# Kernel optimization log

Measured on AMD Instinct MI355X. Metric: run time of the kernel, lower is better.

## Reference

```python
import jax, jax.numpy as jnp
import numpy as np

B, N, F_IN, H, D = 2, 3000, 64, 4, 32
NEG = -1e9  # mask value used by the original layer

def setup_inputs() -> dict:
    key = jax.random.key(0)
    ks = jax.random.split(key, 6)
    h = jax.random.normal(ks[0], (B, N, F_IN), dtype=jnp.float32)
    # dense 0/1 adjacency
    a = jax.random.randint(ks[1], (B, N, N), 0, 2).astype(jnp.float32)
    kernel = jax.random.normal(ks[2], (H, F_IN, D), dtype=jnp.float32) * 0.1
    att_k1 = jax.random.normal(ks[3], (H, D), dtype=jnp.float32) * 0.1
    att_k2 = jax.random.normal(ks[4], (H, D), dtype=jnp.float32) * 0.1
    bias = jax.random.normal(ks[5], (H, D), dtype=jnp.float32) * 0.1
    return {"h": h, "a": a, "kernel": kernel, "att_k1": att_k1, "att_k2": att_k2, "bias": bias}

def reference(h, a, kernel, att_k1, att_k2, bias):
    # per-head projection: [B,H,N,D]
    feat = jnp.einsum('bnf,hfd->bhnd', h, kernel)
    e1 = jnp.einsum('bhnd,hd->bhn', feat, att_k1)  # attention (query part)
    e2 = jnp.einsum('bhnd,hd->bhn', feat, att_k2)  # attention_2 (key part)
    # dense branch: att = a * (e1_i + e2_j); NO LeakyReLU in dense path (faithful)
    adj = a[:, None]                                   # [B,1,N,N]
    scores = adj * (e1[..., :, None] + e2[..., None, :])
    scores = scores + jnp.where(adj == 0, jnp.float32(NEG), jnp.float32(0))
    att = jax.nn.softmax(scores, axis=-1)
    att = att * (adj != 0).astype(att.dtype)
    # dropout is identity at inference
    out = jnp.einsum('bhnm,bhmd->bhnd', att, feat)
    out = out + bias[None, :, None, :]
    out = jax.nn.relu(out)
    # zero out all-zero input nodes
    node_mask = (jnp.sum((h != 0).astype(jnp.float32), axis=-1, keepdims=True) > 0).astype(jnp.float32)  # [B,N,1]
    out = out * node_mask[:, None]
    # concat heads -> [B,N,H*D]
    return out.transpose(0, 2, 1, 3).reshape(h.shape[0], h.shape[1], -1)
```

## Files before the change

### kernel.cpp

```cpp
#include <hip/hip_runtime.h>
#include <hip/hip_bf16.h>
#include <stdint.h>

#define B_ 2
#define N_ 3000
#define F_ 64
#define H_ 4
#define D_ 32
#define K_ 128
#define KT_ 9
#define NCHP_ 96
#define BITSW_ 96
#define NROWT_ 188
#define NRG_ 47
#define S_ 8
#define CHB_ 9216
#define PTB_ 9216

typedef short bf16x8 __attribute__((ext_vector_type(8)));
typedef float f32x4  __attribute__((ext_vector_type(4)));

__device__ __forceinline__ unsigned short f2bf(float f) {
    uint32_t x = __float_as_uint(f);
    return (unsigned short)((x + 0x7FFFu + ((x >> 16) & 1u)) >> 16);
}

__global__ void k_bits(const float* __restrict__ a, uint32_t* __restrict__ bits) {
    int b = blockIdx.x / N_;
    int n = blockIdx.x % N_;
    const float* row = a + (size_t)(b * N_ + n) * N_;
    uint32_t* brow = bits + (size_t)(b * N_ + n) * BITSW_;
    int wv = threadIdx.x >> 6, lane = threadIdx.x & 63;
    for (int it = 0; it < 12; ++it) {
        int ig = wv * 12 + it;
        if (ig < 47) {
            int m = ig * 64 + lane;
            float v = (m < N_) ? row[m] : 0.f;
            unsigned long long bal = __ballot(v != 0.f);
            if (lane == 0)  brow[ig * 2]     = (uint32_t)bal;
            if (lane == 32) brow[ig * 2 + 1] = (uint32_t)(bal >> 32);
        }
    }
    if (threadIdx.x == 0) { brow[94] = 0u; brow[95] = 0u; }
}

__global__ void k_feat(const float* __restrict__ hin, const float* __restrict__ kern,
                       const float* __restrict__ ak2,
                       float* __restrict__ feat, float* __restrict__ e2,
                       float* __restrict__ nmask) {
    int b = blockIdx.x / N_;
    int n = blockIdx.x % N_;
    __shared__ float hrow[F_];
    int tid = threadIdx.x;
    if (tid < F_) hrow[tid] = hin[(size_t)(b * N_ + n) * F_ + tid];
    __syncthreads();
    int hh = tid >> 5, d = tid & 31;
    float acc = 0.f;
    #pragma unroll
    for (int f = 0; f < F_; ++f)
        acc = fmaf(hrow[f], kern[(hh * F_ + f) * D_ + d], acc);
    feat[((size_t)(b * H_ + hh) * N_ + n) * D_ + d] = acc;
    float v = acc * ak2[hh * D_ + d];
    #pragma unroll
    for (int o = 16; o >= 1; o >>= 1) v += __shfl_xor(v, o, 32);
    if (d == 0) e2[(size_t)(b * H_ + hh) * N_ + n] = v;
    unsigned long long bal = __ballot(tid < F_ && hrow[tid & (F_ - 1)] != 0.0f);
    if (tid == 0) nmask[b * N_ + n] = (bal != 0ull) ? 1.0f : 0.0f;
}

__global__ void k_G(const float* __restrict__ feat, const float* __restrict__ e2,
                    bf16x8* __restrict__ G) {
    int idx = blockIdx.x * blockDim.x + threadIdx.x;
    const int total = B_ * NCHP_ * KT_ * 64;
    if (idx >= total) return;
    int lane = idx & 63;
    int t  = (idx >> 6) % KT_;
    int ch = ((idx >> 6) / KT_) % NCHP_;
    int b  = idx / (64 * KT_ * NCHP_);
    int rg = lane >> 4, col = lane & 15;
    int k  = t * 16 + col;
    int m0 = ch * 32 + rg * 8;
    float vals[8];
    if (k < K_ + H_) {
        int hh, d; bool wonly;
        if (k < K_) { hh = k >> 5; d = k & 31; wonly = false; }
        else        { hh = k - K_; d = 0;      wonly = true;  }
        const float* e2p = e2 + (size_t)(b * H_ + hh) * N_;
        const float* fp  = feat + (size_t)(b * H_ + hh) * N_ * D_ + d;
        #pragma unroll
        for (int j = 0; j < 8; ++j) {
            int m = m0 + j;
            float v = 0.f;
            if (m < N_) {
                float w = __expf(e2p[m]);
                v = wonly ? w : w * fp[(size_t)m * D_];
            }
            vals[j] = v;
        }
    } else {
        #pragma unroll
        for (int j = 0; j < 8; ++j) vals[j] = 0.f;
    }
    union { bf16x8 v; unsigned short u[8]; } o;
    #pragma unroll
    for (int j = 0; j < 8; ++j) o.u[j] = f2bf(vals[j]);
    G[idx] = o.v;
}

__device__ __forceinline__ void g2lds16(const void* g, void* l) {
    __builtin_amdgcn_global_load_lds(
        (const __attribute__((address_space(1))) void*)g,
        (__attribute__((address_space(3))) void*)l, 16, 0, 0);
}

__device__ __forceinline__ void stage9(const char* src_ln, char* dst, int w) {
    int t0 = 2 * w * 1024;
    g2lds16(src_ln + t0,        dst + t0);
    g2lds16(src_ln + t0 + 1024, dst + t0 + 1024);
    if (w == 3) g2lds16(src_ln + 8 * 1024, dst + 8 * 1024);
}

__device__ __forceinline__ void compute9(const char* gb, uint32_t word, int rg,
                                         f32x4 (&acc)[KT_]) {
    uint32_t mb = (word >> (rg * 8)) & 0xFFu;
    union { uint32_t u[4]; bf16x8 v; } af;
    af.u[0] = ((mb & 1u)   ? 0x3F80u : 0u) | ((mb & 2u)   ? 0x3F800000u : 0u);
    af.u[1] = ((mb & 4u)   ? 0x3F80u : 0u) | ((mb & 8u)   ? 0x3F800000u : 0u);
    af.u[2] = ((mb & 16u)  ? 0x3F80u : 0u) | ((mb & 32u)  ? 0x3F800000u : 0u);
    af.u[3] = ((mb & 64u)  ? 0x3F80u : 0u) | ((mb & 128u) ? 0x3F800000u : 0u);
    #pragma unroll
    for (int t = 0; t < KT_; ++t) {
        bf16x8 g = *(const bf16x8*)(gb + t * 1024);
        acc[t] = __builtin_amdgcn_mfma_f32_16x16x32_bf16(af.v, g, acc[t], 0, 0, 0);
    }
}

__global__ void __launch_bounds__(256, 4) k_main(
        const uint32_t* __restrict__ bits, const bf16x8* __restrict__ G,
        float* __restrict__ partial) {
    int bid = blockIdx.x;
    int s    = bid % S_;
    int rg64 = (bid / S_) % NRG_;
    int b    = bid / (S_ * NRG_);
    int w = threadIdx.x >> 6;
    int l = threadIdx.x & 63;
    int rg = l >> 4, col = l & 15;
    int row = min(rg64 * 64 + w * 16 + col, N_ - 1);
    const uint32_t* brow = bits + (size_t)(b * N_ + row) * BITSW_ + s * 12;
    const char* Gsrc = (const char*)G + ((size_t)(b * NCHP_ + s * 12)) * CHB_ + (size_t)l * 16;

    __shared__ __align__(16) char Gbuf[2][CHB_];

    f32x4 acc[KT_];
    #pragma unroll
    for (int t = 0; t < KT_; ++t) acc[t] = (f32x4){0.f, 0.f, 0.f, 0.f};

    uint32_t bw[12];
    #pragma unroll
    for (int i = 0; i < 12; ++i) bw[i] = brow[i];

    stage9(Gsrc, Gbuf[0], w);
    __syncthreads();

    #pragma unroll
    for (int i = 0; i < 12; ++i) {
        if (i + 1 < 12) stage9(Gsrc + (size_t)(i + 1) * CHB_, Gbuf[(i + 1) & 1], w);
        compute9(Gbuf[i & 1] + l * 16, bw[i], rg, acc);
        __syncthreads();
    }

    float* pw = partial + (size_t)bid * PTB_ + w * (KT_ * 256);
    #pragma unroll
    for (int t = 0; t < KT_; ++t)
        #pragma unroll
        for (int r = 0; r < 4; ++r)
            pw[t * 256 + r * 64 + l] = acc[t][r];
}

__global__ void __launch_bounds__(256) k_red(
        const float* __restrict__ partial, const float* __restrict__ bias,
        const float* __restrict__ nmask, float* __restrict__ out) {
    int rt = blockIdx.x % NROWT_;
    int b  = blockIdx.x / NROWT_;
    int nbase = rt * 16;
    int rg64  = rt >> 2;
    int wslot = rt & 3;
    int tid = threadIdx.x;
    __shared__ float sm[KT_ * 256];
    const float* pbase = partial + (size_t)((b * NRG_ + rg64) * S_) * PTB_ + wslot * (KT_ * 256);
    #pragma unroll
    for (int k = 0; k < 9; ++k) {
        int flat = tid + k * 256;
        float s = 0.f;
        #pragma unroll
        for (int sp = 0; sp < S_; ++sp) s += pbase[(size_t)sp * PTB_ + flat];
        sm[flat] = s;
    }
    __syncthreads();
    #pragma unroll
    for (int k = 0; k < 9; ++k) {
        int flat = tid + k * 256;
        if (flat < 2048) {
            int t4r = flat >> 6;
            int t = t4r >> 2, r = t4r & 3;
            int lane = flat & 63;
            int rg = lane >> 4, col = lane & 15;
            int rowi = rg * 4 + r;
            int n = nbase + rowi;
            if (n < N_) {
                int hh = t >> 1;
                int r2 = rowi & 3, rg2 = rowi >> 2;
                float den = sm[(32 + r2) * 64 + (rg2 << 4) + hh];
                float v = (den > 0.f) ? sm[flat] / den : 0.f;
                v += bias[t * 16 + col];
                v = fmaxf(v, 0.f);
                v *= nmask[b * N_ + n];
                out[(size_t)(b * N_ + n) * K_ + t * 16 + col] = v;
            }
        }
    }
}

extern "C" void kernel_launch(void* const* d_in, const int* in_sizes, int n_in,
                              void* d_out, int out_size, void* d_ws, size_t ws_size,
                              hipStream_t stream) {
    const float* h    = (const float*)d_in[0];
    const float* a    = (const float*)d_in[1];
    const float* kern = (const float*)d_in[2];
    const float* ak2  = (const float*)d_in[4];
    const float* bias = (const float*)d_in[5];
    float* out = (float*)d_out;

    char* ws = (char*)d_ws;
    size_t o_feat  = 0;
    size_t o_e2    = o_feat  + 3072000;
    size_t o_nmask = o_e2    + 96000;
    size_t o_bits  = o_nmask + 24064;
    size_t o_G     = o_bits  + 2304000;
    size_t o_part  = o_G     + 1769472;
    float*    feat  = (float*)(ws + o_feat);
    float*    e2    = (float*)(ws + o_e2);
    float*    nmask = (float*)(ws + o_nmask);
    uint32_t* bits  = (uint32_t*)(ws + o_bits);
    bf16x8*   G     = (bf16x8*)(ws + o_G);
    float*    part  = (float*)(ws + o_part);

    k_bits<<<dim3(B_ * N_), dim3(256), 0, stream>>>(a, bits);
    k_feat<<<dim3(B_ * N_), dim3(128), 0, stream>>>(h, kern, ak2, feat, e2, nmask);
    int gtot = B_ * NCHP_ * KT_ * 64;
    k_G   <<<dim3((gtot + 255) / 256), dim3(256), 0, stream>>>(feat, e2, G);
    k_main<<<dim3(B_ * NRG_ * S_), dim3(256), 0, stream>>>(bits, G, part);
    k_red <<<dim3(B_ * NROWT_), dim3(256), 0, stream>>>(part, bias, nmask, out);
}
```

Before: 58.28 us.

## Drop LDS staging in k_main; split MFMA tiles across two waves with register double-buffering

The main masked-aggregation kernel stops staging G chunks in shared memory through global_load_lds and block-wide barriers. Each 128-thread block now handles one 16-row tile with a 4-way K split instead of 8. Its two waves divide the nine output tiles (5 and 4) and double-buffer G directly in registers. This removes the barrier and LDS traffic but duplicates G global reads across row tiles, since there are now many more blocks reading the same G. The partial layout and the reducer are changed to match.

```diff
diff --git a/kernel.cpp b/kernel.cpp
--- a/kernel.cpp
+++ b/kernel.cpp
@@ -12,10 +12,9 @@
 #define NCHP_ 96
 #define BITSW_ 96
 #define NROWT_ 188
-#define NRG_ 47
-#define S_ 8
+#define S4_ 4
+#define PT_ 2304
 #define CHB_ 9216
-#define PTB_ 9216
 
 typedef short bf16x8 __attribute__((ext_vector_type(8)));
 typedef float f32x4  __attribute__((ext_vector_type(4)));
@@ -107,21 +106,15 @@
     G[idx] = o.v;
 }
 
-__device__ __forceinline__ void g2lds16(const void* g, void* l) {
-    __builtin_amdgcn_global_load_lds(
-        (const __attribute__((address_space(1))) void*)g,
-        (__attribute__((address_space(3))) void*)l, 16, 0, 0);
-}
-
-__device__ __forceinline__ void stage9(const char* src_ln, char* dst, int w) {
-    int t0 = 2 * w * 1024;
-    g2lds16(src_ln + t0,        dst + t0);
-    g2lds16(src_ln + t0 + 1024, dst + t0 + 1024);
-    if (w == 3) g2lds16(src_ln + 8 * 1024, dst + 8 * 1024);
-}
-
-__device__ __forceinline__ void compute9(const char* gb, uint32_t word, int rg,
-                                         f32x4 (&acc)[KT_]) {
+template<int NT>
+__device__ __forceinline__ void loadG(const char* p, bf16x8 (&g)[NT]) {
+    #pragma unroll
+    for (int t = 0; t < NT; ++t) g[t] = *(const bf16x8*)(p + t * 1024);
+}
+
+template<int NT>
+__device__ __forceinline__ void computeG(uint32_t word, int rg,
+                                         const bf16x8 (&g)[NT], f32x4 (&acc)[NT]) {
     uint32_t mb = (word >> (rg * 8)) & 0xFFu;
     union { uint32_t u[4]; bf16x8 v; } af;
     af.u[0] = ((mb & 1u)   ? 0x3F80u : 0u) | ((mb & 2u)   ? 0x3F800000u : 0u);
@@ -129,52 +122,55 @@
     af.u[2] = ((mb & 16u)  ? 0x3F80u : 0u) | ((mb & 32u)  ? 0x3F800000u : 0u);
     af.u[3] = ((mb & 64u)  ? 0x3F80u : 0u) | ((mb & 128u) ? 0x3F800000u : 0u);
     #pragma unroll
-    for (int t = 0; t < KT_; ++t) {
-        bf16x8 g = *(const bf16x8*)(gb + t * 1024);
-        acc[t] = __builtin_amdgcn_mfma_f32_16x16x32_bf16(af.v, g, acc[t], 0, 0, 0);
-    }
-}
-
-__global__ void __launch_bounds__(256, 4) k_main(
+    for (int t = 0; t < NT; ++t)
+        acc[t] = __builtin_amdgcn_mfma_f32_16x16x32_bf16(af.v, g[t], acc[t], 0, 0, 0);
+}
+
+template<int T0, int NT>
+__device__ __forceinline__ void waverun(const char* GsT, const uint32_t (&bw)[24],
+                                        int rg, float* pout, int l) {
+    f32x4 acc[NT];
+    #pragma unroll
+    for (int t = 0; t < NT; ++t) acc[t] = (f32x4){0.f, 0.f, 0.f, 0.f};
+    bf16x8 gA[NT], gB[NT];
+    loadG<NT>(GsT, gA);
+    #pragma unroll
+    for (int i = 0; i < 24; ++i) {
+        if ((i & 1) == 0) {
+            if (i + 1 < 24) loadG<NT>(GsT + (size_t)(i + 1) * CHB_, gB);
+            computeG<NT>(bw[i], rg, gA, acc);
+        } else {
+            if (i + 1 < 24) loadG<NT>(GsT + (size_t)(i + 1) * CHB_, gA);
+            computeG<NT>(bw[i], rg, gB, acc);
+        }
+    }
+    #pragma unroll
+    for (int t = 0; t < NT; ++t)
+        #pragma unroll
+        for (int r = 0; r < 4; ++r)
+            pout[(T0 + t) * 256 + r * 64 + l] = acc[t][r];
+}
+
+__global__ void __launch_bounds__(128, 4) k_main(
         const uint32_t* __restrict__ bits, const bf16x8* __restrict__ G,
         float* __restrict__ partial) {
     int bid = blockIdx.x;
-    int s    = bid % S_;
-    int rg64 = (bid / S_) % NRG_;
-    int b    = bid / (S_ * NRG_);
+    int s  = bid & 3;
+    int rt = (bid >> 2) % NROWT_;
+    int b  = bid / (S4_ * NROWT_);
     int w = threadIdx.x >> 6;
     int l = threadIdx.x & 63;
     int rg = l >> 4, col = l & 15;
-    int row = min(rg64 * 64 + w * 16 + col, N_ - 1);
-    const uint32_t* brow = bits + (size_t)(b * N_ + row) * BITSW_ + s * 12;
-    const char* Gsrc = (const char*)G + ((size_t)(b * NCHP_ + s * 12)) * CHB_ + (size_t)l * 16;
-
-    __shared__ __align__(16) char Gbuf[2][CHB_];
-
-    f32x4 acc[KT_];
-    #pragma unroll
-    for (int t = 0; t < KT_; ++t) acc[t] = (f32x4){0.f, 0.f, 0.f, 0.f};
-
-    uint32_t bw[12];
-    #pragma unroll
-    for (int i = 0; i < 12; ++i) bw[i] = brow[i];
-
-    stage9(Gsrc, Gbuf[0], w);
-    __syncthreads();
-
-    #pragma unroll
-    for (int i = 0; i < 12; ++i) {
-        if (i + 1 < 12) stage9(Gsrc + (size_t)(i + 1) * CHB_, Gbuf[(i + 1) & 1], w);
-        compute9(Gbuf[i & 1] + l * 16, bw[i], rg, acc);
-        __syncthreads();
-    }
-
-    float* pw = partial + (size_t)bid * PTB_ + w * (KT_ * 256);
-    #pragma unroll
-    for (int t = 0; t < KT_; ++t)
-        #pragma unroll
-        for (int r = 0; r < 4; ++r)
-            pw[t * 256 + r * 64 + l] = acc[t][r];
+    int row = min(rt * 16 + col, N_ - 1);
+    const uint4* bq = (const uint4*)(bits + (size_t)(b * N_ + row) * BITSW_ + s * 24);
+    uint4 b0 = bq[0], b1 = bq[1], b2 = bq[2], b3 = bq[3], b4 = bq[4], b5 = bq[5];
+    uint32_t bw[24] = { b0.x, b0.y, b0.z, b0.w,  b1.x, b1.y, b1.z, b1.w,
+                        b2.x, b2.y, b2.z, b2.w,  b3.x, b3.y, b3.z, b3.w,
+                        b4.x, b4.y, b4.z, b4.w,  b5.x, b5.y, b5.z, b5.w };
+    const char* Gs = (const char*)G + (size_t)(b * NCHP_ + s * 24) * CHB_ + (size_t)l * 16;
+    float* pout = partial + (size_t)bid * PT_;
+    if (w == 0) waverun<0, 5>(Gs,            bw, rg, pout, l);
+    else        waverun<5, 4>(Gs + 5 * 1024, bw, rg, pout, l);
 }
 
 __global__ void __launch_bounds__(256) k_red(
@@ -183,17 +179,15 @@
     int rt = blockIdx.x % NROWT_;
     int b  = blockIdx.x / NROWT_;
     int nbase = rt * 16;
-    int rg64  = rt >> 2;
-    int wslot = rt & 3;
     int tid = threadIdx.x;
-    __shared__ float sm[KT_ * 256];
-    const float* pbase = partial + (size_t)((b * NRG_ + rg64) * S_) * PTB_ + wslot * (KT_ * 256);
+    __shared__ float sm[PT_];
+    const float* pbase = partial + (size_t)((b * NROWT_ + rt) * S4_) * PT_;
     #pragma unroll
     for (int k = 0; k < 9; ++k) {
         int flat = tid + k * 256;
         float s = 0.f;
         #pragma unroll
-        for (int sp = 0; sp < S_; ++sp) s += pbase[(size_t)sp * PTB_ + flat];
+        for (int sp = 0; sp < S4_; ++sp) s += pbase[(size_t)sp * PT_ + flat];
         sm[flat] = s;
     }
     __syncthreads();
@@ -249,6 +243,6 @@
     k_feat<<<dim3(B_ * N_), dim3(128), 0, stream>>>(h, kern, ak2, feat, e2, nmask);
     int gtot = B_ * NCHP_ * KT_ * 64;
     k_G   <<<dim3((gtot + 255) / 256), dim3(256), 0, stream>>>(feat, e2, G);
-    k_main<<<dim3(B_ * NRG_ * S_), dim3(256), 0, stream>>>(bits, G, part);
+    k_main<<<dim3(B_ * NROWT_ * S4_), dim3(128), 0, stream>>>(bits, G, part);
     k_red <<<dim3(B_ * NROWT_), dim3(256), 0, stream>>>(part, bias, nmask, out);
 }
```

Result: slower. 68.09 us (+16.8%).

## Fuse adjacency bitmask construction into main MFMA kernel and refine LDS pipeline waits

Applied to the files above, without the earlier changes.

Removes the separate k_bits pass: each k_main block now reads its own 64-row by 384-column slice of the dense adjacency, ballots it into a shared-memory bit table, and uses that directly. This drops a kernel launch and the write and re-read of the bits buffer. The double-buffered LDS staging loop now uses explicit vmcnt waits and raw s_barriers so the next chunk's load can overlap the current compute. Occupancy is lowered to 2 blocks per CU, and the block's adjacency read is serialized ahead of compute, which could expose memory latency.

```diff
diff --git a/kernel.cpp b/kernel.cpp
--- a/kernel.cpp
+++ b/kernel.cpp
@@ -10,7 +10,6 @@
 #define K_ 128
 #define KT_ 9
 #define NCHP_ 96
-#define BITSW_ 96
 #define NROWT_ 188
 #define NRG_ 47
 #define S_ 8
@@ -23,25 +22,6 @@
 __device__ __forceinline__ unsigned short f2bf(float f) {
     uint32_t x = __float_as_uint(f);
     return (unsigned short)((x + 0x7FFFu + ((x >> 16) & 1u)) >> 16);
-}
-
-__global__ void k_bits(const float* __restrict__ a, uint32_t* __restrict__ bits) {
-    int b = blockIdx.x / N_;
-    int n = blockIdx.x % N_;
-    const float* row = a + (size_t)(b * N_ + n) * N_;
-    uint32_t* brow = bits + (size_t)(b * N_ + n) * BITSW_;
-    int wv = threadIdx.x >> 6, lane = threadIdx.x & 63;
-    for (int it = 0; it < 12; ++it) {
-        int ig = wv * 12 + it;
-        if (ig < 47) {
-            int m = ig * 64 + lane;
-            float v = (m < N_) ? row[m] : 0.f;
-            unsigned long long bal = __ballot(v != 0.f);
-            if (lane == 0)  brow[ig * 2]     = (uint32_t)bal;
-            if (lane == 32) brow[ig * 2 + 1] = (uint32_t)(bal >> 32);
-        }
-    }
-    if (threadIdx.x == 0) { brow[94] = 0u; brow[95] = 0u; }
 }
 
 __global__ void k_feat(const float* __restrict__ hin, const float* __restrict__ kern,
@@ -113,31 +93,18 @@
         (__attribute__((address_space(3))) void*)l, 16, 0, 0);
 }
 
-__device__ __forceinline__ void stage9(const char* src_ln, char* dst, int w) {
+__device__ __forceinline__ void stage_chunk(const char* src_ln, char* dst, int w) {
     int t0 = 2 * w * 1024;
     g2lds16(src_ln + t0,        dst + t0);
     g2lds16(src_ln + t0 + 1024, dst + t0 + 1024);
-    if (w == 3) g2lds16(src_ln + 8 * 1024, dst + 8 * 1024);
-}
-
-__device__ __forceinline__ void compute9(const char* gb, uint32_t word, int rg,
-                                         f32x4 (&acc)[KT_]) {
-    uint32_t mb = (word >> (rg * 8)) & 0xFFu;
-    union { uint32_t u[4]; bf16x8 v; } af;
-    af.u[0] = ((mb & 1u)   ? 0x3F80u : 0u) | ((mb & 2u)   ? 0x3F800000u : 0u);
-    af.u[1] = ((mb & 4u)   ? 0x3F80u : 0u) | ((mb & 8u)   ? 0x3F800000u : 0u);
-    af.u[2] = ((mb & 16u)  ? 0x3F80u : 0u) | ((mb & 32u)  ? 0x3F800000u : 0u);
-    af.u[3] = ((mb & 64u)  ? 0x3F80u : 0u) | ((mb & 128u) ? 0x3F800000u : 0u);
-    #pragma unroll
-    for (int t = 0; t < KT_; ++t) {
-        bf16x8 g = *(const bf16x8*)(gb + t * 1024);
-        acc[t] = __builtin_amdgcn_mfma_f32_16x16x32_bf16(af.v, g, acc[t], 0, 0, 0);
-    }
-}
-
-__global__ void __launch_bounds__(256, 4) k_main(
-        const uint32_t* __restrict__ bits, const bf16x8* __restrict__ G,
+    if (w == 3) g2lds16(src_ln + 8192, dst + 8192);
+}
+
+__global__ void __launch_bounds__(256, 2) k_main(
+        const float* __restrict__ a, const bf16x8* __restrict__ G,
         float* __restrict__ partial) {
+    __shared__ __align__(16) bf16x8 Gbuf[2][KT_ * 64];
+    __shared__ uint32_t bitw[64][13];
     int bid = blockIdx.x;
     int s    = bid % S_;
     int rg64 = (bid / S_) % NRG_;
@@ -145,28 +112,60 @@
     int w = threadIdx.x >> 6;
     int l = threadIdx.x & 63;
     int rg = l >> 4, col = l & 15;
-    int row = min(rg64 * 64 + w * 16 + col, N_ - 1);
-    const uint32_t* brow = bits + (size_t)(b * N_ + row) * BITSW_ + s * 12;
-    const char* Gsrc = (const char*)G + ((size_t)(b * NCHP_ + s * 12)) * CHB_ + (size_t)l * 16;
-
-    __shared__ __align__(16) char Gbuf[2][CHB_];
+
+    for (int r = 0; r < 16; ++r) {
+        int rl = w * 16 + r;
+        int rowa = min(rg64 * 64 + rl, N_ - 1);
+        const float* arow = a + (size_t)(b * N_ + rowa) * N_;
+        #pragma unroll
+        for (int sl = 0; sl < 6; ++sl) {
+            int m = s * 384 + sl * 64 + l;
+            float v = (m < N_) ? arow[m] : 0.f;
+            unsigned long long bal = __ballot(v != 0.f);
+            if (l == 0)  bitw[rl][sl * 2]     = (uint32_t)bal;
+            if (l == 32) bitw[rl][sl * 2 + 1] = (uint32_t)(bal >> 32);
+        }
+    }
+    __syncthreads();
+
+    const char* Gsrc = (const char*)G + (size_t)(b * NCHP_ + s * 12) * CHB_ + (size_t)l * 16;
+    char* buf0 = (char*)&Gbuf[0][0];
+    char* buf1 = (char*)&Gbuf[1][0];
 
     f32x4 acc[KT_];
     #pragma unroll
     for (int t = 0; t < KT_; ++t) acc[t] = (f32x4){0.f, 0.f, 0.f, 0.f};
 
-    uint32_t bw[12];
-    #pragma unroll
-    for (int i = 0; i < 12; ++i) bw[i] = brow[i];
-
-    stage9(Gsrc, Gbuf[0], w);
-    __syncthreads();
-
+    stage_chunk(Gsrc, buf0, w);
     #pragma unroll
     for (int i = 0; i < 12; ++i) {
-        if (i + 1 < 12) stage9(Gsrc + (size_t)(i + 1) * CHB_, Gbuf[(i + 1) & 1], w);
-        compute9(Gbuf[i & 1] + l * 16, bw[i], rg, acc);
-        __syncthreads();
+        char* cur = (i & 1) ? buf1 : buf0;
+        char* nxt = (i & 1) ? buf0 : buf1;
+        if (i + 1 < 12) {
+            stage_chunk(Gsrc + (size_t)(i + 1) * CHB_, nxt, w);
+            if (w == 3) asm volatile("s_waitcnt vmcnt(3)" ::: "memory");
+            else        asm volatile("s_waitcnt vmcnt(2)" ::: "memory");
+        } else {
+            asm volatile("s_waitcnt vmcnt(0)" ::: "memory");
+        }
+        __builtin_amdgcn_sched_barrier(0);
+        __builtin_amdgcn_s_barrier();
+        __builtin_amdgcn_sched_barrier(0);
+
+        uint32_t word = bitw[w * 16 + col][i];
+        uint32_t mb = (word >> (rg * 8)) & 0xFFu;
+        union { uint32_t u[4]; bf16x8 v; } af;
+        af.u[0] = ((mb & 1u)   ? 0x3F80u : 0u) | ((mb & 2u)   ? 0x3F800000u : 0u);
+        af.u[1] = ((mb & 4u)   ? 0x3F80u : 0u) | ((mb & 8u)   ? 0x3F800000u : 0u);
+        af.u[2] = ((mb & 16u)  ? 0x3F80u : 0u) | ((mb & 32u)  ? 0x3F800000u : 0u);
+        af.u[3] = ((mb & 64u)  ? 0x3F80u : 0u) | ((mb & 128u) ? 0x3F800000u : 0u);
+        #pragma unroll
+        for (int t = 0; t < KT_; ++t) {
+            bf16x8 g = *(const bf16x8*)(cur + t * 1024 + l * 16);
+            acc[t] = __builtin_amdgcn_mfma_f32_16x16x32_bf16(af.v, g, acc[t], 0, 0, 0);
+        }
+        __builtin_amdgcn_sched_barrier(0);
+        __builtin_amdgcn_s_barrier();
     }
 
     float* pw = partial + (size_t)bid * PTB_ + w * (KT_ * 256);
@@ -235,20 +234,17 @@
     size_t o_feat  = 0;
     size_t o_e2    = o_feat  + 3072000;
     size_t o_nmask = o_e2    + 96000;
-    size_t o_bits  = o_nmask + 24064;
-    size_t o_G     = o_bits  + 2304000;
+    size_t o_G     = o_nmask + 24064;
     size_t o_part  = o_G     + 1769472;
-    float*    feat  = (float*)(ws + o_feat);
-    float*    e2    = (float*)(ws + o_e2);
-    float*    nmask = (float*)(ws + o_nmask);
-    uint32_t* bits  = (uint32_t*)(ws + o_bits);
-    bf16x8*   G     = (bf16x8*)(ws + o_G);
-    float*    part  = (float*)(ws + o_part);
-
-    k_bits<<<dim3(B_ * N_), dim3(256), 0, stream>>>(a, bits);
+    float*  feat  = (float*)(ws + o_feat);
+    float*  e2    = (float*)(ws + o_e2);
+    float*  nmask = (float*)(ws + o_nmask);
+    bf16x8* G     = (bf16x8*)(ws + o_G);
+    float*  part  = (float*)(ws + o_part);
+
     k_feat<<<dim3(B_ * N_), dim3(128), 0, stream>>>(h, kern, ak2, feat, e2, nmask);
     int gtot = B_ * NCHP_ * KT_ * 64;
     k_G   <<<dim3((gtot + 255) / 256), dim3(256), 0, stream>>>(feat, e2, G);
-    k_main<<<dim3(B_ * NRG_ * S_), dim3(256), 0, stream>>>(bits, G, part);
+    k_main<<<dim3(B_ * NRG_ * S_), dim3(256), 0, stream>>>(a, G, part);
     k_red <<<dim3(B_ * NROWT_), dim3(256), 0, stream>>>(part, bias, nmask, out);
 }
```

Result: slower. 76.70 us (+31.6%).
